# Performance work log

Hardware: AMD Instinct MI355X
Metric: run time of the kernel (lower is better)

Reference implementation:

```python
import jax, jax.numpy as jnp
import numpy as np

B, N, DEG = 256, 16384, 32  # batch, num_neurons, fan-in per neuron

def setup_inputs() -> dict:
    key = jax.random.key(0)
    kx, kw, ki = jax.random.split(key, 3)
    x = jax.random.normal(kx, (B, N), dtype=jnp.float32)
    w = jax.random.normal(kw, (N, DEG), dtype=jnp.float32)  # nonzero weights per neuron
    idx = jax.random.randint(ki, (N, DEG), 0, N)            # source-neuron indices per neuron
    return {"x": x, "w": w, "idx": idx}

def reference(x, w, idx):
    # Per neuron j: gather its fan-in channels and apply Dense(1) with
    # kernel = nonzero weights, then relu; concat over neurons == axis N.
    gathered = x[:, idx]                      # [B, N, DEG] gather
    out = jnp.einsum('bnd,nd->bn', gathered, w)  # sparse matvec per batch row
    return jax.nn.relu(out)                   # [B, N]
```

## Files before the change

kernel.cpp:

```cpp
#include <hip/hip_runtime.h>


#define NB   16384
#define DEG  32

typedef __fp16 hp2 __attribute__((ext_vector_type(2)));

__global__ __launch_bounds__(256) void prep_pw_kernel(
    const int* __restrict__ idx, const float* __restrict__ w,
    uint2* __restrict__ pw) {
    __shared__ int   idx_s[64][33];
    __shared__ float w_s[64][33];
    const int t  = threadIdx.x;
    const int nb = blockIdx.x * 64;

    const int4*   src  = (const int4*)(idx + (size_t)nb * DEG);
    const float4* srcw = (const float4*)(w   + (size_t)nb * DEG);
#pragma unroll
    for (int p = 0; p < 2; ++p) {
        const int e4 = t + 256 * p;
        const int n0 = e4 >> 3;
        const int c0 = (e4 & 7) * 4;
        const int4 v = src[e4];
        idx_s[n0][c0 + 0] = v.x; idx_s[n0][c0 + 1] = v.y;
        idx_s[n0][c0 + 2] = v.z; idx_s[n0][c0 + 3] = v.w;
        const float4 f = srcw[e4];
        w_s[n0][c0 + 0] = f.x; w_s[n0][c0 + 1] = f.y;
        w_s[n0][c0 + 2] = f.z; w_s[n0][c0 + 3] = f.w;
    }
    __syncthreads();

    const int np    = t & 63;
    const int dbase = t >> 6;
#pragma unroll
    for (int k = 0; k < 4; ++k) {
        const int d2 = dbase * 4 + k;
        const unsigned j0 = (unsigned)idx_s[np][2 * d2];
        const unsigned j1 = (unsigned)idx_s[np][2 * d2 + 1];
        const hp2 wp = __builtin_amdgcn_cvt_pkrtz(w_s[np][2 * d2], w_s[np][2 * d2 + 1]);
        uint2 o;
        o.x = j0 | (j1 << 16);
        o.y = __builtin_bit_cast(unsigned, wp);
        pw[(size_t)d2 * NB + nb + np] = o;
    }
}

__global__ __launch_bounds__(512) void fused_gather_kernel(
    const float* __restrict__ x, const uint2* __restrict__ pw,
    float* __restrict__ out) {
    __shared__ unsigned xh[NB];
    const int t    = threadIdx.x;
    const int bg   = (int)blockIdx.x >> 1;
    const int half = (int)blockIdx.x & 1;
    const int b0   = bg * 2;
    const float* xr0 = x + (size_t)b0 * NB;
    const float* xr1 = xr0 + NB;

#pragma unroll
    for (int p = 0; p < 8; ++p) {
        const int j = 4 * (t + 512 * p);
        const float4 a0 = *(const float4*)&xr0[j];
        const float4 a1 = *(const float4*)&xr1[j];
        uint4 o;
        o.x = __builtin_bit_cast(unsigned, (hp2)__builtin_amdgcn_cvt_pkrtz(a0.x, a1.x));
        o.y = __builtin_bit_cast(unsigned, (hp2)__builtin_amdgcn_cvt_pkrtz(a0.y, a1.y));
        o.z = __builtin_bit_cast(unsigned, (hp2)__builtin_amdgcn_cvt_pkrtz(a0.z, a1.z));
        o.w = __builtin_bit_cast(unsigned, (hp2)__builtin_amdgcn_cvt_pkrtz(a0.w, a1.w));
        *(uint4*)&xh[j] = o;
    }
    __syncthreads();

    const int nbase = half * 8192;
#pragma unroll 2
    for (int i = 0; i < 16; ++i) {
        const int n = nbase + t + 512 * i;
        uint2 q[16];
#pragma unroll
        for (int d2 = 0; d2 < 16; ++d2)
            q[d2] = pw[(size_t)d2 * NB + n];

        float acc0 = 0.f, acc1 = 0.f;
#pragma unroll
        for (int d2 = 0; d2 < 16; ++d2) {
            const unsigned jp = q[d2].x;
            const unsigned r0 = xh[jp & 0xffffu];
            const unsigned r1 = xh[jp >> 16];
            const hp2 w2 = __builtin_bit_cast(hp2, q[d2].y);
            const hp2 p0 = __builtin_bit_cast(hp2, r0);
            const hp2 p1 = __builtin_bit_cast(hp2, r1);
            acc0 = fmaf((float)w2.x, (float)p0.x, acc0);
            acc1 = fmaf((float)w2.x, (float)p0.y, acc1);
            acc0 = fmaf((float)w2.y, (float)p1.x, acc0);
            acc1 = fmaf((float)w2.y, (float)p1.y, acc1);
        }
        out[(size_t)b0 * NB + n]       = fmaxf(acc0, 0.f);
        out[(size_t)(b0 + 1) * NB + n] = fmaxf(acc1, 0.f);
    }
}

extern "C" void kernel_launch(void* const* d_in, const int* in_sizes, int n_in,
                              void* d_out, int out_size, void* d_ws, size_t ws_size,
                              hipStream_t stream) {
    const float* x   = (const float*)d_in[0];
    const float* w   = (const float*)d_in[1];
    const int*   idx = (const int*)d_in[2];
    float* out = (float*)d_out;
    uint2* pw  = (uint2*)d_ws;

    prep_pw_kernel<<<NB / 64, 256, 0, stream>>>(idx, w, pw);

    fused_gather_kernel<<<256, 512, 0, stream>>>(x, pw, out);
}
```

Baseline: 96.67 us.

## Pack four batch rows per LDS entry and accumulate in packed fp16

Moves the fp32-to-fp16 conversion of x into the prep kernel, writing a packed layout with four batch rows per 8-byte entry. The gather kernel then stages 128KB of packed x in LDS per block and processes four batch rows per gathered index. This halves the number of LDS gathers and pw reloads per output. Accumulation switches from fp32 FMAs to packed fp16 adds/multiplies split into two partial sums, trading accuracy for fewer ALU ops. It also adds an extra global round trip for the packed x and needs 128KB of dynamic LDS.

```diff
diff --git a/kernel.cpp b/kernel.cpp
--- a/kernel.cpp
+++ b/kernel.cpp
@@ -6,14 +6,35 @@
 
 typedef __fp16 hp2 __attribute__((ext_vector_type(2)));
 
-__global__ __launch_bounds__(256) void prep_pw_kernel(
+__device__ __forceinline__ unsigned pk16(float a, float b) {
+    return __builtin_bit_cast(unsigned, (hp2)__builtin_amdgcn_cvt_pkrtz(a, b));
+}
+
+__global__ __launch_bounds__(256) void prep_kernel(
     const int* __restrict__ idx, const float* __restrict__ w,
-    uint2* __restrict__ pw) {
+    const float* __restrict__ x, uint2* __restrict__ pw,
+    uint2* __restrict__ xq) {
     __shared__ int   idx_s[64][33];
     __shared__ float w_s[64][33];
-    const int t  = threadIdx.x;
-    const int nb = blockIdx.x * 64;
+    const int t = threadIdx.x;
 
+    if (blockIdx.x < 4096) {
+        const int jt = (int)blockIdx.x & 63;
+        const int q  = (int)blockIdx.x >> 6;
+        const int j  = jt * 256 + t;
+        const float* xr = x + (size_t)(4 * q) * NB + j;
+        const float a0 = xr[0];
+        const float a1 = xr[NB];
+        const float a2 = xr[2 * NB];
+        const float a3 = xr[3 * NB];
+        uint2 o;
+        o.x = pk16(a0, a1);
+        o.y = pk16(a2, a3);
+        xq[((size_t)q << 14) + j] = o;
+        return;
+    }
+
+    const int nb = ((int)blockIdx.x - 4096) * 64;
     const int4*   src  = (const int4*)(idx + (size_t)nb * DEG);
     const float4* srcw = (const float4*)(w   + (size_t)nb * DEG);
 #pragma unroll
@@ -35,66 +56,70 @@
 #pragma unroll
     for (int k = 0; k < 4; ++k) {
         const int d2 = dbase * 4 + k;
-        const unsigned j0 = (unsigned)idx_s[np][2 * d2];
-        const unsigned j1 = (unsigned)idx_s[np][2 * d2 + 1];
-        const hp2 wp = __builtin_amdgcn_cvt_pkrtz(w_s[np][2 * d2], w_s[np][2 * d2 + 1]);
         uint2 o;
-        o.x = j0 | (j1 << 16);
-        o.y = __builtin_bit_cast(unsigned, wp);
+        o.x = (unsigned)idx_s[np][2 * d2] | ((unsigned)idx_s[np][2 * d2 + 1] << 16);
+        o.y = pk16(w_s[np][2 * d2], w_s[np][2 * d2 + 1]);
         pw[(size_t)d2 * NB + nb + np] = o;
     }
 }
 
-__global__ __launch_bounds__(512) void fused_gather_kernel(
-    const float* __restrict__ x, const uint2* __restrict__ pw,
+__global__ __launch_bounds__(1024) void gather4_kernel(
+    const uint2* __restrict__ xq, const uint2* __restrict__ pw,
     float* __restrict__ out) {
-    __shared__ unsigned xh[NB];
-    const int t    = threadIdx.x;
-    const int bg   = (int)blockIdx.x >> 1;
-    const int half = (int)blockIdx.x & 1;
-    const int b0   = bg * 2;
-    const float* xr0 = x + (size_t)b0 * NB;
-    const float* xr1 = xr0 + NB;
+    extern __shared__ uint2 lds[];
+    const int t  = threadIdx.x;
+    const int q  = (int)blockIdx.x >> 2;
+    const int n0 = ((int)blockIdx.x & 3) * 4096;
 
+    {
+        const uint4* src = (const uint4*)(xq + ((size_t)q << 14));
+        uint4* dst = (uint4*)lds;
 #pragma unroll
-    for (int p = 0; p < 8; ++p) {
-        const int j = 4 * (t + 512 * p);
-        const float4 a0 = *(const float4*)&xr0[j];
-        const float4 a1 = *(const float4*)&xr1[j];
-        uint4 o;
-        o.x = __builtin_bit_cast(unsigned, (hp2)__builtin_amdgcn_cvt_pkrtz(a0.x, a1.x));
-        o.y = __builtin_bit_cast(unsigned, (hp2)__builtin_amdgcn_cvt_pkrtz(a0.y, a1.y));
-        o.z = __builtin_bit_cast(unsigned, (hp2)__builtin_amdgcn_cvt_pkrtz(a0.z, a1.z));
-        o.w = __builtin_bit_cast(unsigned, (hp2)__builtin_amdgcn_cvt_pkrtz(a0.w, a1.w));
-        *(uint4*)&xh[j] = o;
+        for (int i = 0; i < 8; ++i) dst[t + 1024 * i] = src[t + 1024 * i];
     }
     __syncthreads();
 
-    const int nbase = half * 8192;
-#pragma unroll 2
-    for (int i = 0; i < 16; ++i) {
-        const int n = nbase + t + 512 * i;
-        uint2 q[16];
+    const int b0 = 4 * q;
+    for (int i = 0; i < 4; ++i) {
+        const int n = n0 + t + 1024 * i;
+        uint2 qd[16];
 #pragma unroll
         for (int d2 = 0; d2 < 16; ++d2)
-            q[d2] = pw[(size_t)d2 * NB + n];
+            qd[d2] = pw[(size_t)d2 * NB + n];
 
-        float acc0 = 0.f, acc1 = 0.f;
+        hp2 a01 = {0, 0}, a23 = {0, 0}, c01 = {0, 0}, c23 = {0, 0};
 #pragma unroll
-        for (int d2 = 0; d2 < 16; ++d2) {
-            const unsigned jp = q[d2].x;
-            const unsigned r0 = xh[jp & 0xffffu];
-            const unsigned r1 = xh[jp >> 16];
-            const hp2 w2 = __builtin_bit_cast(hp2, q[d2].y);
-            const hp2 p0 = __builtin_bit_cast(hp2, r0);
-            const hp2 p1 = __builtin_bit_cast(hp2, r1);
-            acc0 = fmaf((float)w2.x, (float)p0.x, acc0);
-            acc1 = fmaf((float)w2.x, (float)p0.y, acc1);
-            acc0 = fmaf((float)w2.y, (float)p1.x, acc0);
-            acc1 = fmaf((float)w2.y, (float)p1.y, acc1);
+        for (int d2 = 0; d2 < 8; ++d2) {
+            const unsigned jp = qd[d2].x;
+            const uint2 g0 = lds[jp & 0xffffu];
+            const uint2 g1 = lds[jp >> 16];
+            const hp2 w2 = __builtin_bit_cast(hp2, qd[d2].y);
+            const hp2 wlo = {w2.x, w2.x};
+            const hp2 whi = {w2.y, w2.y};
+            a01 += wlo * __builtin_bit_cast(hp2, g0.x);
+            a23 += wlo * __builtin_bit_cast(hp2, g0.y);
+            a01 += whi * __builtin_bit_cast(hp2, g1.x);
+            a23 += whi * __builtin_bit_cast(hp2, g1.y);
         }
-        out[(size_t)b0 * NB + n]       = fmaxf(acc0, 0.f);
-        out[(size_t)(b0 + 1) * NB + n] = fmaxf(acc1, 0.f);
+#pragma unroll
+        for (int d2 = 8; d2 < 16; ++d2) {
+            const unsigned jp = qd[d2].x;
+            const uint2 g0 = lds[jp & 0xffffu];
+            const uint2 g1 = lds[jp >> 16];
+            const hp2 w2 = __builtin_bit_cast(hp2, qd[d2].y);
+            const hp2 wlo = {w2.x, w2.x};
+            const hp2 whi = {w2.y, w2.y};
+            c01 += wlo * __builtin_bit_cast(hp2, g0.x);
+            c23 += wlo * __builtin_bit_cast(hp2, g0.y);
+            c01 += whi * __builtin_bit_cast(hp2, g1.x);
+            c23 += whi * __builtin_bit_cast(hp2, g1.y);
+        }
+        const hp2 s01 = a01 + c01;
+        const hp2 s23 = a23 + c23;
+        out[(size_t)(b0 + 0) * NB + n] = fmaxf((float)s01.x, 0.f);
+        out[(size_t)(b0 + 1) * NB + n] = fmaxf((float)s01.y, 0.f);
+        out[(size_t)(b0 + 2) * NB + n] = fmaxf((float)s23.x, 0.f);
+        out[(size_t)(b0 + 3) * NB + n] = fmaxf((float)s23.y, 0.f);
     }
 }
 
@@ -106,8 +131,12 @@
     const int*   idx = (const int*)d_in[2];
     float* out = (float*)d_out;
     uint2* pw  = (uint2*)d_ws;
+    uint2* xq  = (uint2*)((char*)d_ws + (2u << 20));
 
-    prep_pw_kernel<<<NB / 64, 256, 0, stream>>>(idx, w, pw);
+    (void)hipFuncSetAttribute((const void*)gather4_kernel,
+                              hipFuncAttributeMaxDynamicSharedMemorySize, 131072);
 
-    fused_gather_kernel<<<256, 512, 0, stream>>>(x, pw, out);
+    prep_kernel<<<4096 + NB / 64, 256, 0, stream>>>(idx, w, x, pw, xq);
+
+    gather4_kernel<<<256, 1024, 131072, stream>>>(xq, pw, out);
 }
```

Result: faster. 90.61 us (-6.3%).
